# Kernel optimization log

Measured on AMD Instinct MI355X. Metric: run time of the kernel, lower is better.

## Reference

```python
import jax, jax.numpy as jnp
import numpy as np

B, S = 32768, 512  # rays, max bright spots (= 2*max_samples)


def setup_inputs() -> dict:
    key = jax.random.key(0)
    k1, k2, k3, k4, k5 = jax.random.split(key, 5)
    V = jax.random.normal(k1, (B, 3), dtype=jnp.float32)
    N = jax.random.normal(k2, (B, 3), dtype=jnp.float32)
    N = N / jnp.linalg.norm(N, axis=-1, keepdims=True)
    spots = jax.random.normal(k3, (S, 3), dtype=jnp.float32)
    spots = spots / jnp.linalg.norm(spots, axis=-1, keepdims=True)
    # prefix masks: num_ele[i] <= num_ray[i] <= S (matches kernel's start_ind-j indexing)
    num_ray = jax.random.randint(k4, (B,), S // 2, S + 1)
    num_ele = jax.random.randint(k5, (B,), 0, S // 2)
    j = jnp.arange(S)
    ray_mask = j[None, :] < num_ray[:, None]
    bright_mask = j[None, :] < num_ele[:, None]
    std = jnp.float32(0.05)  # pix_size
    return {"V": V, "N": N, "spots": spots, "ray_mask": ray_mask,
            "bright_mask": bright_mask, "std": std}


def reference(V, N, spots, ray_mask, bright_mask, std):
    Bn, Sn = bright_mask.shape
    # wp.randf(seed): uniform in [0,1), one per written component -> (B,S,3)
    u = jax.random.uniform(jax.random.key(42), (Bn, Sn, 3), dtype=spots.dtype)
    num_ele = bright_mask.sum(axis=1)            # n per row
    num_ray = ray_mask.sum(axis=1)               # start_ind = num_ray - 1
    j = jnp.arange(Sn)
    active = j[None, :] < num_ele[:, None]       # j in range(n)
    jit = spots[None, :, :] + std * u            # jittered light dirs (B,S,3)
    LdotN = jnp.einsum('bsd,bd->bs', jit, N)
    cond = active & (LdotN > 0.0)                # rejection test
    t = num_ray[:, None] - 1 - j[None, :]        # reversed write index
    t_safe = jnp.where(cond & (t >= 0) & (t < Sn), t, Sn)  # Sn -> dropped
    b_idx = jnp.arange(Bn)[:, None]
    Ls = jnp.zeros((Bn, Sn, 3), spots.dtype).at[b_idx, t_safe].set(jit, mode='drop')
    bmask = jnp.zeros((Bn, Sn), jnp.int32).at[b_idx, t_safe].set(1, mode='drop')
    return Ls, bmask.astype(bool)
```

## Files before the change

kernel.cpp:

```cpp
#include <hip/hip_runtime.h>


#define TF_ROUND(x0, x1, r) { x0 += x1; x1 = ((x1 << (r)) | (x1 >> (32 - (r)))); x1 ^= x0; }

__device__ __forceinline__ unsigned tf2x32_seed42_xor(unsigned x0, unsigned x1) {
  const unsigned k0 = 0u, k1 = 42u;
  const unsigned k2 = 0x1BD11BDAu ^ k0 ^ k1;
  x0 += k0; x1 += k1;
  TF_ROUND(x0,x1,13) TF_ROUND(x0,x1,15) TF_ROUND(x0,x1,26) TF_ROUND(x0,x1,6)
  x0 += k1; x1 += k2 + 1u;
  TF_ROUND(x0,x1,17) TF_ROUND(x0,x1,29) TF_ROUND(x0,x1,16) TF_ROUND(x0,x1,24)
  x0 += k2; x1 += k0 + 2u;
  TF_ROUND(x0,x1,13) TF_ROUND(x0,x1,15) TF_ROUND(x0,x1,26) TF_ROUND(x0,x1,6)
  x0 += k0; x1 += k1 + 3u;
  TF_ROUND(x0,x1,17) TF_ROUND(x0,x1,29) TF_ROUND(x0,x1,16) TF_ROUND(x0,x1,24)
  x0 += k1; x1 += k2 + 4u;
  TF_ROUND(x0,x1,13) TF_ROUND(x0,x1,15) TF_ROUND(x0,x1,26) TF_ROUND(x0,x1,6)
  x0 += k2; x1 += k0 + 5u;
  return x0 ^ x1;
}

typedef float f4v __attribute__((ext_vector_type(4)));

__device__ __forceinline__ int detect_mode(const unsigned char* m) {
  const unsigned char d0 = m[0], d1 = m[1], d4 = m[4];
  return (d0 == 0) ? 3 : ((d1 != 0) ? 0 : ((d4 != 0) ? 1 : 2));
}

__global__ __launch_bounds__(256, 8) void bis_row4(
    const float* __restrict__ Nrm, const float* __restrict__ spots,
    const unsigned char* __restrict__ rmask, const unsigned char* __restrict__ emask,
    const float* __restrict__ stdp, float* __restrict__ Ls, float* __restrict__ bm,
    int B)
{
  const int tid = threadIdx.x;
  const int w = tid >> 6;
  const int l = tid & 63;
  const int b = blockIdx.x * 4 + w;
  if (b >= B) return;

  __shared__ f4v s_jit[4][256];

  const int mode = detect_mode(rmask);
  const unsigned base = (unsigned)b * 512u + (unsigned)(l << 3);

  int rcnt = 0, ecnt = 0;
  if (mode == 0) {
    const uint2 rv = *(const uint2*)(rmask + base);
    const uint2 ev = *(const uint2*)(emask + base);
    rcnt = __popc(rv.x & 0x01010101u) + __popc(rv.y & 0x01010101u);
    ecnt = __popc(ev.x & 0x01010101u) + __popc(ev.y & 0x01010101u);
  } else if (mode == 1) {
    const int* rp = (const int*)rmask + base; const int* ep = (const int*)emask + base;
    const int4 r0 = *(const int4*)rp, r1 = *(const int4*)(rp + 4);
    const int4 e0 = *(const int4*)ep, e1 = *(const int4*)(ep + 4);
    rcnt = (r0.x!=0)+(r0.y!=0)+(r0.z!=0)+(r0.w!=0)+(r1.x!=0)+(r1.y!=0)+(r1.z!=0)+(r1.w!=0);
    ecnt = (e0.x!=0)+(e0.y!=0)+(e0.z!=0)+(e0.w!=0)+(e1.x!=0)+(e1.y!=0)+(e1.z!=0)+(e1.w!=0);
  } else if (mode == 3) {
    const float* rp = (const float*)rmask + base; const float* ep = (const float*)emask + base;
    const float4 r0 = *(const float4*)rp, r1 = *(const float4*)(rp + 4);
    const float4 e0 = *(const float4*)ep, e1 = *(const float4*)(ep + 4);
    rcnt = (r0.x!=0.f)+(r0.y!=0.f)+(r0.z!=0.f)+(r0.w!=0.f)+(r1.x!=0.f)+(r1.y!=0.f)+(r1.z!=0.f)+(r1.w!=0.f);
    ecnt = (e0.x!=0.f)+(e0.y!=0.f)+(e0.z!=0.f)+(e0.w!=0.f)+(e1.x!=0.f)+(e1.y!=0.f)+(e1.z!=0.f)+(e1.w!=0.f);
  } else {
    const long long* rp = (const long long*)rmask; const long long* ep = (const long long*)emask;
    #pragma unroll
    for (int c = 0; c < 8; ++c) { rcnt += rp[base+c] != 0; ecnt += ep[base+c] != 0; }
  }
  unsigned pack = (unsigned)rcnt | ((unsigned)ecnt << 16);
  #pragma unroll
  for (int off = 1; off < 64; off <<= 1) pack += __shfl_xor(pack, off, 64);
  const int num_ray = (int)(pack & 0xFFFFu);
  const int num_ele = (int)(pack >> 16);

  if (num_ele > 0) {
    const float stdv = stdp[0];
    const float n0 = Nrm[b*3+0], n1 = Nrm[b*3+1], n2 = Nrm[b*3+2];
    for (int j = l; j < num_ele; j += 64) {
      const unsigned f = ((unsigned)b * 512u + (unsigned)j) * 3u;
      const float u0 = __uint_as_float((tf2x32_seed42_xor(0u, f + 0u) >> 9) | 0x3F800000u) - 1.0f;
      const float u1 = __uint_as_float((tf2x32_seed42_xor(0u, f + 1u) >> 9) | 0x3F800000u) - 1.0f;
      const float u2 = __uint_as_float((tf2x32_seed42_xor(0u, f + 2u) >> 9) | 0x3F800000u) - 1.0f;
      const float j0 = __fadd_rn(spots[j*3+0], __fmul_rn(stdv, u0));
      const float j1 = __fadd_rn(spots[j*3+1], __fmul_rn(stdv, u1));
      const float j2 = __fadd_rn(spots[j*3+2], __fmul_rn(stdv, u2));
      const float d  = __fadd_rn(__fadd_rn(__fmul_rn(j0,n0), __fmul_rn(j1,n1)),
                                 __fmul_rn(j2,n2));
      const bool acc = (d > 0.0f);
      f4v e; e.x = acc ? j0 : 0.f; e.y = acc ? j1 : 0.f; e.z = acc ? j2 : 0.f;
      e.w = acc ? 1.f : 0.f;
      s_jit[w][j] = e;
    }
  }
  asm volatile("s_waitcnt lgkmcnt(0)" ::: "memory");

  const int lo = num_ray - num_ele;
  const int hi = num_ray;
  const float* jrow = (const float*)&s_jit[w][0];

  f4v* lsrow = (f4v*)(Ls + (size_t)b * 1536u);
  #pragma unroll
  for (int i = 0; i < 6; ++i) {
    const int g = i * 64 + l;
    const unsigned ff0 = (unsigned)(g << 2);
    const int s0 = (int)((ff0 * 43691u) >> 17);
    const int s1 = (int)(((ff0 + 3u) * 43691u) >> 17);
    f4v o = {0.f, 0.f, 0.f, 0.f};
    if (s1 >= lo && s0 < hi) {
      #pragma unroll
      for (int k = 0; k < 4; ++k) {
        const unsigned ff = ff0 + (unsigned)k;
        const unsigned s  = (ff * 43691u) >> 17;
        const unsigned comp = ff - 3u * s;
        const int jj = num_ray - 1 - (int)s;
        if (jj >= 0 && jj < num_ele) o[k] = jrow[(unsigned)jj * 4u + comp];
      }
    }
    lsrow[g] = o;
  }

  f4v* bmrow = (f4v*)(bm + (size_t)b * 512u);
  #pragma unroll
  for (int i = 0; i < 2; ++i) {
    const int g = i * 64 + l;
    const int sb = g << 2;
    f4v o = {0.f, 0.f, 0.f, 0.f};
    if (sb + 3 >= lo && sb < hi) {
      #pragma unroll
      for (int k = 0; k < 4; ++k) {
        const int jj = num_ray - 1 - (sb + k);
        if (jj >= 0 && jj < num_ele) o[k] = jrow[(unsigned)jj * 4u + 3u];
      }
    }
    bmrow[g] = o;
  }
}

struct F3 { float x, y, z; };

__global__ __launch_bounds__(512) void bis_kernel_s(
    const float* __restrict__ Nrm, const float* __restrict__ spots,
    const unsigned char* __restrict__ rmask, const unsigned char* __restrict__ emask,
    const float* __restrict__ stdp, float* __restrict__ Ls, float* __restrict__ bm,
    int S)
{
  const long long b = blockIdx.x;
  const int t = threadIdx.x;
  const int mode = detect_mode(rmask);

  const long long e = b * (long long)S + t;
  int rnz, enz;
  if (mode == 0)      { rnz = rmask[e] != 0;                     enz = emask[e] != 0; }
  else if (mode == 1) { rnz = ((const int*)rmask)[e] != 0;       enz = ((const int*)emask)[e] != 0; }
  else if (mode == 2) { rnz = ((const long long*)rmask)[e] != 0; enz = ((const long long*)emask)[e] != 0; }
  else                { rnz = ((const float*)rmask)[e] != 0.0f;  enz = ((const float*)emask)[e] != 0.0f; }

  __shared__ int s_nr[16], s_ne[16];
  const unsigned long long br = __ballot(rnz);
  const unsigned long long be = __ballot(enz);
  const int w = t >> 6;
  if ((t & 63) == 0) { s_nr[w] = __popcll(br); s_ne[w] = __popcll(be); }
  __syncthreads();
  const int nw = blockDim.x >> 6;
  int num_ray = 0, num_ele = 0;
  for (int i = 0; i < nw; ++i) { num_ray += s_nr[i]; num_ele += s_ne[i]; }

  const int j = num_ray - 1 - t;
  float o0 = 0.f, o1 = 0.f, o2 = 0.f, m = 0.f;
  if (j >= 0 && j < num_ele) {
    const float stdv = stdp[0];
    const float n0 = Nrm[b*3+0], n1 = Nrm[b*3+1], n2 = Nrm[b*3+2];
    const unsigned f = (unsigned)((b * (long long)S + j) * 3LL);
    const float u0 = __uint_as_float((tf2x32_seed42_xor(0u, f + 0u) >> 9) | 0x3F800000u) - 1.0f;
    const float u1 = __uint_as_float((tf2x32_seed42_xor(0u, f + 1u) >> 9) | 0x3F800000u) - 1.0f;
    const float u2 = __uint_as_float((tf2x32_seed42_xor(0u, f + 2u) >> 9) | 0x3F800000u) - 1.0f;
    const float j0 = __fadd_rn(spots[j*3+0], __fmul_rn(stdv, u0));
    const float j1 = __fadd_rn(spots[j*3+1], __fmul_rn(stdv, u1));
    const float j2 = __fadd_rn(spots[j*3+2], __fmul_rn(stdv, u2));
    const float d  = __fadd_rn(__fadd_rn(__fmul_rn(j0,n0), __fmul_rn(j1,n1)), __fmul_rn(j2,n2));
    if (d > 0.0f) { o0 = j0; o1 = j1; o2 = j2; m = 1.0f; }
  }

  const long long oidx = b * (long long)S + t;
  F3 v; v.x = o0; v.y = o1; v.z = o2;
  reinterpret_cast<F3*>(Ls)[oidx] = v;
  bm[oidx] = m;
}

extern "C" void kernel_launch(void* const* d_in, const int* in_sizes, int n_in,
                              void* d_out, int out_size, void* d_ws, size_t ws_size,
                              hipStream_t stream) {
  const float* Nrm = (const float*)d_in[1];
  const float* spots = (const float*)d_in[2];
  const unsigned char* rmask = (const unsigned char*)d_in[3];
  const unsigned char* emask = (const unsigned char*)d_in[4];
  const float* stdp = (const float*)d_in[5];

  const int B = in_sizes[0] / 3;
  const int S = in_sizes[2] / 3;

  float* out = (float*)d_out;
  float* Ls = out;
  float* bm = out + (long long)B * S * 3;

  if (S == 512) {
    dim3 grid((unsigned)((B + 3) / 4)), block(256);
    hipLaunchKernelGGL(bis_row4, grid, block, 0, stream,
                       Nrm, spots, rmask, emask, stdp, Ls, bm, B);
  } else {
    dim3 grid((unsigned)B), block((unsigned)S);
    hipLaunchKernelGGL(bis_kernel_s, grid, block, 0, stream,
                       Nrm, spots, rmask, emask, stdp, Ls, bm, S);
  }
}
```

Measured before the change: 84.26 us.

## Scatter jittered spots into a zeroed shared row image, then copy out

Each wave now zeroes a full 2048-float row image in shared memory and scatters accepted jittered spots directly to their reversed output positions, along with the mask flag. The output is then a straight vector copy from LDS to global, replacing the per-element index arithmetic (divide-by-3 tricks, range checks, gathers). Shared memory per block grows from 16KB to 32KB and the occupancy hint drops from 8 to 4 blocks. The scattered scalar LDS writes may hit bank conflicts.

```diff
diff --git a/kernel.cpp b/kernel.cpp
--- a/kernel.cpp
+++ b/kernel.cpp
@@ -27,7 +27,7 @@
   return (d0 == 0) ? 3 : ((d1 != 0) ? 0 : ((d4 != 0) ? 1 : 2));
 }
 
-__global__ __launch_bounds__(256, 8) void bis_row4(
+__global__ __launch_bounds__(256, 4) void bis_direct(
     const float* __restrict__ Nrm, const float* __restrict__ spots,
     const unsigned char* __restrict__ rmask, const unsigned char* __restrict__ emask,
     const float* __restrict__ stdp, float* __restrict__ Ls, float* __restrict__ bm,
@@ -39,7 +39,8 @@
   const int b = blockIdx.x * 4 + w;
   if (b >= B) return;
 
-  __shared__ f4v s_jit[4][256];
+  __shared__ f4v s_row[4][512];
+  float* rowf = (float*)&s_row[w][0];
 
   const int mode = detect_mode(rmask);
   const unsigned base = (unsigned)b * 512u + (unsigned)(l << 3);
@@ -73,6 +74,12 @@
   const int num_ray = (int)(pack & 0xFFFFu);
   const int num_ele = (int)(pack >> 16);
 
+  {
+    const f4v z = {0.f, 0.f, 0.f, 0.f};
+    #pragma unroll
+    for (int i = 0; i < 8; ++i) s_row[w][i * 64 + l] = z;
+  }
+
   if (num_ele > 0) {
     const float stdv = stdp[0];
     const float n0 = Nrm[b*3+0], n1 = Nrm[b*3+1], n2 = Nrm[b*3+2];
@@ -86,53 +93,28 @@
       const float j2 = __fadd_rn(spots[j*3+2], __fmul_rn(stdv, u2));
       const float d  = __fadd_rn(__fadd_rn(__fmul_rn(j0,n0), __fmul_rn(j1,n1)),
                                  __fmul_rn(j2,n2));
-      const bool acc = (d > 0.0f);
-      f4v e; e.x = acc ? j0 : 0.f; e.y = acc ? j1 : 0.f; e.z = acc ? j2 : 0.f;
-      e.w = acc ? 1.f : 0.f;
-      s_jit[w][j] = e;
+      if (d > 0.0f) {
+        const int t = num_ray - 1 - j;
+        rowf[3*t + 0] = j0;
+        rowf[3*t + 1] = j1;
+        rowf[3*t + 2] = j2;
+        rowf[1536 + t] = 1.0f;
+      }
     }
   }
   asm volatile("s_waitcnt lgkmcnt(0)" ::: "memory");
-
-  const int lo = num_ray - num_ele;
-  const int hi = num_ray;
-  const float* jrow = (const float*)&s_jit[w][0];
 
   f4v* lsrow = (f4v*)(Ls + (size_t)b * 1536u);
   #pragma unroll
   for (int i = 0; i < 6; ++i) {
     const int g = i * 64 + l;
-    const unsigned ff0 = (unsigned)(g << 2);
-    const int s0 = (int)((ff0 * 43691u) >> 17);
-    const int s1 = (int)(((ff0 + 3u) * 43691u) >> 17);
-    f4v o = {0.f, 0.f, 0.f, 0.f};
-    if (s1 >= lo && s0 < hi) {
-      #pragma unroll
-      for (int k = 0; k < 4; ++k) {
-        const unsigned ff = ff0 + (unsigned)k;
-        const unsigned s  = (ff * 43691u) >> 17;
-        const unsigned comp = ff - 3u * s;
-        const int jj = num_ray - 1 - (int)s;
-        if (jj >= 0 && jj < num_ele) o[k] = jrow[(unsigned)jj * 4u + comp];
-      }
-    }
-    lsrow[g] = o;
+    lsrow[g] = s_row[w][g];
   }
-
   f4v* bmrow = (f4v*)(bm + (size_t)b * 512u);
   #pragma unroll
   for (int i = 0; i < 2; ++i) {
     const int g = i * 64 + l;
-    const int sb = g << 2;
-    f4v o = {0.f, 0.f, 0.f, 0.f};
-    if (sb + 3 >= lo && sb < hi) {
-      #pragma unroll
-      for (int k = 0; k < 4; ++k) {
-        const int jj = num_ray - 1 - (sb + k);
-        if (jj >= 0 && jj < num_ele) o[k] = jrow[(unsigned)jj * 4u + 3u];
-      }
-    }
-    bmrow[g] = o;
+    bmrow[g] = s_row[w][384 + g];
   }
 }
 
@@ -205,7 +187,7 @@
 
   if (S == 512) {
     dim3 grid((unsigned)((B + 3) / 4)), block(256);
-    hipLaunchKernelGGL(bis_row4, grid, block, 0, stream,
+    hipLaunchKernelGGL(bis_direct, grid, block, 0, stream,
                        Nrm, spots, rmask, emask, stdp, Ls, bm, B);
   } else {
     dim3 grid((unsigned)B), block((unsigned)S);
```

Result: slower. 87.49 us (+3.8%).
